# Kernel tuning notes

Measured on AMD Instinct MI355X. Metric: run time of the kernel, lower is better.

Reference implementation:

```python
import jax, jax.numpy as jnp
import numpy as np

VOCAB, D_MODEL, NHEAD, NLAYER, DIM_FF, MAX_LEN = 32000, 1024, 16, 6, 4096, 1024
B, L = 8, 1024
PAD_ID = 0
EPS = 1e-5


def _ln(x, g, b):
    m = x.mean(-1, keepdims=True)
    v = x.var(-1, keepdims=True)
    return (x - m) / jnp.sqrt(v + EPS) * g + b


def _mha(x, Wqkv, bqkv, Wo, bo, kpm):
    # x: [B,L,D]; Wqkv: [3D,D]; kpm: [B,L] bool (True = padded key)
    Bx, Lx, D = x.shape
    dh = D // NHEAD
    qkv = x @ Wqkv.T + bqkv                       # [B,L,3D]
    q, k, v = jnp.split(qkv, 3, axis=-1)
    sp = lambda t: t.reshape(Bx, Lx, NHEAD, dh).transpose(0, 2, 1, 3)  # [B,H,L,dh]
    q, k, v = sp(q), sp(k), sp(v)
    scores = jnp.einsum('bhqd,bhkd->bhqk', q, k) * (dh ** -0.5)
    scores = jnp.where(kpm[:, None, None, :], jnp.asarray(-1e9, scores.dtype), scores)
    attn = jax.nn.softmax(scores, axis=-1)        # explicit weights, as ForceWeightsMHA demands
    o = jnp.einsum('bhqk,bhkd->bhqd', attn, v)
    o = o.transpose(0, 2, 1, 3).reshape(Bx, Lx, D)
    return o @ Wo.T + bo


def setup_inputs() -> dict:
    key = jax.random.key(0)
    ks = jax.random.split(key, 20)
    s = 0.02
    n = lambda k, shp: (jax.random.normal(k, shp, dtype=jnp.float32) * s)
    inp = {
        'input_ids': jax.random.randint(ks[0], (B, L), 0, VOCAB, dtype=jnp.int64) if jax.config.jax_enable_x64 else jax.random.randint(ks[0], (B, L), 0, VOCAB).astype(jnp.int32),
        'tok_emb': n(ks[1], (VOCAB, D_MODEL)),
        'pos_emb': n(ks[2], (MAX_LEN, D_MODEL)),
        'Wqkv': n(ks[3], (NLAYER, 3 * D_MODEL, D_MODEL)),
        'bqkv': jnp.zeros((NLAYER, 3 * D_MODEL), jnp.float32),
        'Wo': n(ks[4], (NLAYER, D_MODEL, D_MODEL)),
        'bo': jnp.zeros((NLAYER, D_MODEL), jnp.float32),
        'ln1_g': jnp.ones((NLAYER, D_MODEL), jnp.float32),
        'ln1_b': jnp.zeros((NLAYER, D_MODEL), jnp.float32),
        'W1': n(ks[5], (NLAYER, DIM_FF, D_MODEL)),
        'b1': jnp.zeros((NLAYER, DIM_FF), jnp.float32),
        'W2': n(ks[6], (NLAYER, D_MODEL, DIM_FF)),
        'b2': jnp.zeros((NLAYER, D_MODEL), jnp.float32),
        'ln2_g': jnp.ones((NLAYER, D_MODEL), jnp.float32),
        'ln2_b': jnp.zeros((NLAYER, D_MODEL), jnp.float32),
        'head_ln_g': jnp.ones((D_MODEL,), jnp.float32),
        'head_ln_b': jnp.zeros((D_MODEL,), jnp.float32),
        'head_W': n(ks[7], (MAX_LEN, D_MODEL)),
        'head_b': jnp.zeros((MAX_LEN,), jnp.float32),
    }
    return inp


def reference(input_ids, tok_emb, pos_emb, Wqkv, bqkv, Wo, bo, ln1_g, ln1_b,
              W1, b1, W2, b2, ln2_g, ln2_b, head_ln_g, head_ln_b, head_W, head_b):
    Bx, Lx = input_ids.shape
    x = tok_emb[input_ids] + pos_emb[None, :Lx]           # [B,L,D]
    kpm = (input_ids == PAD_ID).at[:, 0].set(False)        # key padding mask, col 0 forced valid
    for i in range(NLAYER):                                # post-norm encoder layer (PyTorch default)
        x = _ln(x + _mha(x, Wqkv[i], bqkv[i], Wo[i], bo[i], kpm), ln1_g[i], ln1_b[i])
        ff = jax.nn.gelu(x @ W1[i].T + b1[i], approximate=False) @ W2[i].T + b2[i]
        x = _ln(x + ff, ln2_g[i], ln2_b[i])
    cls = x[:, 0, :]                                       # [B,D]
    return _ln(cls, head_ln_g, head_ln_b) @ head_W.T + head_b  # [B,MAX_LEN]
```

## Files before the change

### kernel.cpp

```cpp
#include <hip/hip_runtime.h>
#include <cstdint>

#define D_MODEL 1024
#define NHEAD   16
#define NLAYER  6
#define DIM_FF  4096
#define SEQ_B   8
#define SEQ_L   1024
#define TOKENS  (SEQ_B*SEQ_L)

typedef __bf16 v8bf  __attribute__((ext_vector_type(8)));
typedef __bf16 v4bf  __attribute__((ext_vector_type(4)));
typedef float  v4f   __attribute__((ext_vector_type(4)));

__device__ __forceinline__ void gl_lds16(const void* g, void* l) {
  __builtin_amdgcn_global_load_lds(
      (const __attribute__((address_space(1))) void*)g,
      (__attribute__((address_space(3))) void*)l, 16, 0, 0);
}

__global__ __launch_bounds__(256) void f2b_kernel(const float4* __restrict__ in,
                                                  ushort4* __restrict__ out, long n4) {
  long i = (long)blockIdx.x * 256 + threadIdx.x;
  long stride = (long)gridDim.x * 256;
  for (; i < n4; i += stride) {
    float4 v = in[i];
    v4bf r = { (__bf16)v.x, (__bf16)v.y, (__bf16)v.z, (__bf16)v.w };
    out[i] = *(ushort4*)&r;
  }
}

__global__ __launch_bounds__(256) void embed_kernel(const int* __restrict__ ids,
    const float4* __restrict__ tok, const float4* __restrict__ pos,
    float4* __restrict__ X, ushort4* __restrict__ Xb) {
  long i = (long)blockIdx.x * 256 + threadIdx.x;
  int d4 = (int)(i & 255);
  long bl = i >> 8;
  int l = (int)(bl & (SEQ_L - 1));
  int id = ids[bl];
  float4 t = tok[(long)id * 256 + d4];
  float4 p = pos[(long)l * 256 + d4];
  float4 v = {t.x + p.x, t.y + p.y, t.z + p.z, t.w + p.w};
  X[i] = v;
  v4bf r = { (__bf16)v.x, (__bf16)v.y, (__bf16)v.z, (__bf16)v.w };
  Xb[i] = *(ushort4*)&r;
}

__global__ __launch_bounds__(256) void maskb_kernel(const int* __restrict__ ids,
                                                    float* __restrict__ mb) {
  int i = blockIdx.x * 256 + threadIdx.x;
  mb[i] = (ids[i] == 0 && (i & 1023) != 0) ? -1e9f : 0.f;
}

template<int EPI>
__global__ __launch_bounds__(256) void gemm128(
    const unsigned short* __restrict__ A,
    const unsigned short* __restrict__ W,
    const float* __restrict__ bias,
    const float* __restrict__ Res,
    float* __restrict__ Cf, unsigned short* __restrict__ Cb,
    unsigned short* __restrict__ Vt,
    int M, int N, int K) {
  __shared__ unsigned short As[2 * 128 * 32];
  __shared__ unsigned short Bs[2 * 128 * 32];
  int tid = threadIdx.x;
  int wave = tid >> 6, lane = tid & 63;
  int l15 = lane & 15, quad = lane >> 4;

  int id = blockIdx.y * gridDim.x + blockIdx.x;
  int xcd = id & 7, sidx = id >> 3;
  int mt = xcd * 8 + (sidx & 7);
  int nt = sidx >> 3;
  int m0 = mt * 128, n0 = nt * 128;
  int wm = (wave >> 1) * 64, wn = (wave & 1) * 64;

  int srow = tid >> 2;
  int ssl  = (tid & 3) ^ ((srow >> 1) & 3);
  int sc8  = ssl << 3;
  const unsigned short* Ag0 = A + (long)(m0 + srow) * K + sc8;
  const unsigned short* Ag1 = A + (long)(m0 + srow + 64) * K + sc8;
  const unsigned short* Wg0 = W + (long)(n0 + srow) * K + sc8;
  const unsigned short* Wg1 = W + (long)(n0 + srow + 64) * K + sc8;
  unsigned short* As0 = As + tid * 8;
  unsigned short* Bs0 = Bs + tid * 8;

  const unsigned short* afp[4];
  const unsigned short* bfp[4];
  #pragma unroll
  for (int i = 0; i < 4; ++i) {
    int r = wm + i * 16 + l15;
    afp[i] = &As[r * 32 + ((quad ^ ((r >> 1) & 3)) << 3)];
    int rb = wn + i * 16 + l15;
    bfp[i] = &Bs[rb * 32 + ((quad ^ ((rb >> 1) & 3)) << 3)];
  }

  v4f acc[4][4];
  #pragma unroll
  for (int i = 0; i < 4; ++i)
    #pragma unroll
    for (int j = 0; j < 4; ++j) acc[i][j] = (v4f){0.f, 0.f, 0.f, 0.f};

  auto compute = [&](int bo) {
    v8bf af[4], bb[4];
    #pragma unroll
    for (int i = 0; i < 4; ++i) af[i] = *(const v8bf*)(afp[i] + bo);
    #pragma unroll
    for (int j = 0; j < 4; ++j) bb[j] = *(const v8bf*)(bfp[j] + bo);
    #pragma unroll
    for (int i = 0; i < 4; ++i)
      #pragma unroll
      for (int j = 0; j < 4; ++j)
        acc[i][j] = __builtin_amdgcn_mfma_f32_16x16x32_bf16(af[i], bb[j], acc[i][j], 0, 0, 0);
  };

  gl_lds16(Ag0, As0);
  gl_lds16(Ag1, As0 + 2048);
  gl_lds16(Wg0, Bs0);
  gl_lds16(Wg1, Bs0 + 2048);

  int ksteps = K >> 5;
  for (int ks = 0; ks < ksteps; ks += 2) {
    __syncthreads();
    {
      int k1 = (ks + 1) << 5;
      gl_lds16(Ag0 + k1, As0 + 4096);
      gl_lds16(Ag1 + k1, As0 + 6144);
      gl_lds16(Wg0 + k1, Bs0 + 4096);
      gl_lds16(Wg1 + k1, Bs0 + 6144);
    }
    compute(0);
    __syncthreads();
    if (ks + 2 < ksteps) {
      int k2 = (ks + 2) << 5;
      gl_lds16(Ag0 + k2, As0);
      gl_lds16(Ag1 + k2, As0 + 2048);
      gl_lds16(Wg0 + k2, Bs0);
      gl_lds16(Wg1 + k2, Bs0 + 2048);
    }
    compute(4096);
  }

  #pragma unroll
  for (int i = 0; i < 4; ++i) {
    int crow0 = m0 + wm + i * 16 + quad * 4;
    #pragma unroll
    for (int j = 0; j < 4; ++j) {
      int col = n0 + wn + j * 16 + l15;
      float bv = bias[col];
      if (EPI == 3 && col >= 2048) {
        int hc = (col - 2048) >> 6, d = (col - 2048) & 63;
        int bb2 = crow0 >> 10, l = crow0 & 1023;
        v4bf pk = { (__bf16)(acc[i][j][0] + bv), (__bf16)(acc[i][j][1] + bv),
                    (__bf16)(acc[i][j][2] + bv), (__bf16)(acc[i][j][3] + bv) };
        *(ushort4*)&Vt[((long)((bb2 * 16 + hc) * 64 + d)) * 1024 + l] = *(ushort4*)&pk;
      } else {
        #pragma unroll
        for (int r = 0; r < 4; ++r) {
          float v = acc[i][j][r] + bv;
          long idx = (long)(crow0 + r) * N + col;
          if (EPI == 1) {
            float u = v * (0.7978845608028654f + 0.03567740814f * v * v);
            float e = __builtin_amdgcn_exp2f(u * 2.885390081777927f);
            float th = 1.f - 2.f / (e + 1.f);
            v = 0.5f * v * (1.f + th);
          }
          if (EPI == 0) Cf[idx] = v + Res[idx];
          else          ((__bf16*)Cb)[idx] = (__bf16)v;
        }
      }
    }
  }
}

#define PSP 72
__global__ __launch_bounds__(256) void attn2(
    const unsigned short* __restrict__ QKVb,
    const unsigned short* __restrict__ Vtg,
    const float* __restrict__ mb,
    unsigned short* __restrict__ Ob) {
  __shared__ unsigned short Ks[2 * 64 * 64];
  __shared__ unsigned short Vs[2 * 64 * 64];
  __shared__ unsigned short Ps[4][16 * PSP];
  int tid = threadIdx.x, wave = tid >> 6, lane = tid & 63;
  int l15 = lane & 15, quad = lane >> 4;
  int b = blockIdx.z, h = blockIdx.y, q0 = blockIdx.x * 128;

  v8bf gq[2][2];
  #pragma unroll
  for (int t = 0; t < 2; ++t) {
    int qrow = q0 + t * 64 + wave * 16 + l15;
    const unsigned short* qb = QKVb + (long)(b * 1024 + qrow) * 3072 + h * 64;
    gq[t][0] = *(const v8bf*)(qb + quad * 8);
    gq[t][1] = *(const v8bf*)(qb + 32 + quad * 8);
  }

  v8bf bones;
  #pragma unroll
  for (int j = 0; j < 8; ++j) bones[j] = (l15 == 0) ? (__bf16)1.0f : (__bf16)0.0f;

  float m_run[2][4], l_run[2][4];
  v4f O[2][4];
  #pragma unroll
  for (int t = 0; t < 2; ++t)
    #pragma unroll
    for (int r = 0; r < 4; ++r) {
      m_run[t][r] = -1e30f; l_run[t][r] = 0.f;
      O[t][r] = (v4f){0.f, 0.f, 0.f, 0.f};
    }

  const unsigned short* kgb = QKVb + (long)b * 1024 * 3072 + 1024 + h * 64;
  const unsigned short* vgb = Vtg + (long)((b * 16 + h) * 64) * 1024;
  const float* mrow = mb + b * 1024;

  int srow = tid >> 3;
  int ssl  = (tid & 7) ^ (srow & 7);
  int ph0 = (quad ^ (l15 & 7)) << 3;
  int ph1 = ((quad + 4) ^ (l15 & 7)) << 3;
  const float SC = 0.18033688011112042f;

  gl_lds16(kgb + (long)srow * 3072 + ssl * 8, &Ks[tid * 8]);
  gl_lds16(kgb + (long)(srow + 32) * 3072 + ssl * 8, &Ks[tid * 8 + 2048]);
  gl_lds16(vgb + (long)srow * 1024 + ssl * 8, &Vs[tid * 8]);
  gl_lds16(vgb + (long)(srow + 32) * 1024 + ssl * 8, &Vs[tid * 8 + 2048]);

  for (int c = 0; c < 16; ++c) {
    int cbo = (c & 1) * 4096;
    __syncthreads();
    if (c + 1 < 16) {
      int nbo = 4096 - cbo;
      int k0n = (c + 1) * 64;
      gl_lds16(kgb + (long)(k0n + srow) * 3072 + ssl * 8, &Ks[nbo + tid * 8]);
      gl_lds16(kgb + (long)(k0n + srow + 32) * 3072 + ssl * 8, &Ks[nbo + tid * 8 + 2048]);
      gl_lds16(vgb + (long)srow * 1024 + k0n + ssl * 8, &Vs[nbo + tid * 8]);
      gl_lds16(vgb + (long)(srow + 32) * 1024 + k0n + ssl * 8, &Vs[nbo + tid * 8 + 2048]);
    }
    int k0 = c * 64;

    v8bf kf0[4], kf1[4];
    #pragma unroll
    for (int t = 0; t < 4; ++t) {
      kf0[t] = *(const v8bf*)&Ks[cbo + (t * 16 + l15) * 64 + ph0];
      kf1[t] = *(const v8bf*)&Ks[cbo + (t * 16 + l15) * 64 + ph1];
    }
    float mbv[4];
    #pragma unroll
    for (int t = 0; t < 4; ++t) mbv[t] = mrow[k0 + t * 16 + l15];

    #pragma unroll
    for (int tt = 0; tt < 2; ++tt) {
      float p[4][4], mr[4];
      #pragma unroll
      for (int r = 0; r < 4; ++r) mr[r] = -1e30f;
      #pragma unroll
      for (int t = 0; t < 4; ++t) {
        v4f s = (v4f){0.f, 0.f, 0.f, 0.f};
        s = __builtin_amdgcn_mfma_f32_16x16x32_bf16(gq[tt][0], kf0[t], s, 0, 0, 0);
        s = __builtin_amdgcn_mfma_f32_16x16x32_bf16(gq[tt][1], kf1[t], s, 0, 0, 0);
        #pragma unroll
        for (int r = 0; r < 4; ++r) {
          float sv = fmaf(s[r], SC, mbv[t]);
          p[t][r] = sv;
          mr[r] = fmaxf(mr[r], sv);
        }
      }
      #pragma unroll
      for (int r = 0; r < 4; ++r) {
        mr[r] = fmaxf(mr[r], __shfl_xor(mr[r], 1, 64));
        mr[r] = fmaxf(mr[r], __shfl_xor(mr[r], 2, 64));
        mr[r] = fmaxf(mr[r], __shfl_xor(mr[r], 4, 64));
        mr[r] = fmaxf(mr[r], __shfl_xor(mr[r], 8, 64));
      }
      float alpha[4];
      #pragma unroll
      for (int r = 0; r < 4; ++r) {
        float mn = fmaxf(m_run[tt][r], mr[r]);
        alpha[r] = __builtin_amdgcn_exp2f(m_run[tt][r] - mn);
        m_run[tt][r] = mn;
      }
      #pragma unroll
      for (int t = 0; t < 4; ++t)
        #pragma unroll
        for (int r = 0; r < 4; ++r)
          p[t][r] = __builtin_amdgcn_exp2f(p[t][r] - m_run[tt][r]);

      #pragma unroll
      for (int t = 0; t < 4; ++t)
        #pragma unroll
        for (int r = 0; r < 4; ++r)
          ((__bf16*)Ps[wave])[(quad * 4 + r) * PSP + t * 16 + l15] = (__bf16)p[t][r];
      v8bf pa0 = *(const v8bf*)&Ps[wave][l15 * PSP + quad * 8];
      v8bf pa1 = *(const v8bf*)&Ps[wave][l15 * PSP + 32 + quad * 8];

      v4f ss = (v4f){0.f, 0.f, 0.f, 0.f};
      ss = __builtin_amdgcn_mfma_f32_16x16x32_bf16(pa0, bones, ss, 0, 0, 0);
      ss = __builtin_amdgcn_mfma_f32_16x16x32_bf16(pa1, bones, ss, 0, 0, 0);

      #pragma unroll
      for (int j = 0; j < 4; ++j)
        #pragma unroll
        for (int r = 0; r < 4; ++r) O[tt][j >= 0 ? j : j][r] *= (j == 0 ? alpha[r] : 1.f);
      #pragma unroll
      for (int j = 1; j < 4; ++j)
        #pragma unroll
        for (int r = 0; r < 4; ++r) O[tt][j][r] *= alpha[r];

      #pragma unroll
      for (int j = 0; j < 4; ++j) {
        v8bf vf0 = *(const v8bf*)&Vs[cbo + (j * 16 + l15) * 64 + ph0];
        v8bf vf1 = *(const v8bf*)&Vs[cbo + (j * 16 + l15) * 64 + ph1];
        O[tt][j] = __builtin_amdgcn_mfma_f32_16x16x32_bf16(pa0, vf0, O[tt][j], 0, 0, 0);
        O[tt][j] = __builtin_amdgcn_mfma_f32_16x16x32_bf16(pa1, vf1, O[tt][j], 0, 0, 0);
      }
      #pragma unroll
      for (int r = 0; r < 4; ++r)
        l_run[tt][r] = l_run[tt][r] * alpha[r] + __shfl(ss[r], quad << 4, 64);
    }
  }

  #pragma unroll
  for (int tt = 0; tt < 2; ++tt) {
    int qd = q0 + tt * 64 + wave * 16 + quad * 4;
    #pragma unroll
    for (int r = 0; r < 4; ++r) {
      float inv = 1.f / l_run[tt][r];
      #pragma unroll
      for (int j = 0; j < 4; ++j)
        ((__bf16*)Ob)[(long)(b * 1024 + qd + r) * 1024 + h * 64 + j * 16 + l15] =
            (__bf16)(O[tt][j][r] * inv);
    }
  }
}

__global__ __launch_bounds__(256) void add_ln(
    const float* __restrict__ Xin, const float* __restrict__ Yin,
    const float* __restrict__ g, const float* __restrict__ bta,
    float* __restrict__ outF, unsigned short* __restrict__ outB,
    long in_stride, long out_stride) {
  int row = blockIdx.x;
  const float* x = Xin + (long)row * in_stride;
  const float* y = Yin ? Yin + (long)row * 1024 : nullptr;
  int tid = threadIdx.x;
  float v[4];
  float s = 0.f, s2 = 0.f;
  #pragma unroll
  for (int j = 0; j < 4; ++j) {
    int d = j * 256 + tid;
    float t = x[d] + (y ? y[d] : 0.f);
    v[j] = t; s += t; s2 += t * t;
  }
  __shared__ float red[8];
  int lane = tid & 63, wave = tid >> 6;
  #pragma unroll
  for (int o = 32; o > 0; o >>= 1) { s += __shfl_down(s, o, 64); s2 += __shfl_down(s2, o, 64); }
  if (lane == 0) { red[wave] = s; red[4 + wave] = s2; }
  __syncthreads();
  s  = red[0] + red[1] + red[2] + red[3];
  s2 = red[4] + red[5] + red[6] + red[7];
  float mean = s * (1.f / 1024.f);
  float var  = s2 * (1.f / 1024.f) - mean * mean;
  float rstd = rsqrtf(var + 1e-5f);
  float* of = outF + (long)row * out_stride;
  unsigned short* ob = outB ? outB + (long)row * out_stride : nullptr;
  #pragma unroll
  for (int j = 0; j < 4; ++j) {
    int d = j * 256 + tid;
    float o = (v[j] - mean) * rstd * g[d] + bta[d];
    of[d] = o;
    if (ob) ((__bf16*)ob)[d] = (__bf16)o;
  }
}

__global__ __launch_bounds__(256) void head_kernel(
    const float* __restrict__ cls, const float* __restrict__ hW,
    const float* __restrict__ hb, float* __restrict__ out) {
  int n = blockIdx.x * 256 + threadIdx.x;
  int b = blockIdx.y;
  const float4* c4 = (const float4*)(cls + b * 1024);
  const float4* w4 = (const float4*)(hW + (long)n * 1024);
  float s = 0.f;
  #pragma unroll 8
  for (int d = 0; d < 256; ++d) {
    float4 a = c4[d], w = w4[d];
    s += a.x * w.x + a.y * w.y + a.z * w.z + a.w * w.w;
  }
  out[b * 1024 + n] = s + hb[n];
}

extern "C" void kernel_launch(void* const* d_in, const int* in_sizes, int n_in,
                              void* d_out, int out_size, void* d_ws, size_t ws_size,
                              hipStream_t stream) {
  const int*   ids  = (const int*)d_in[0];
  const float* tok  = (const float*)d_in[1];
  const float* pos  = (const float*)d_in[2];
  const float* Wqkv = (const float*)d_in[3];
  const float* bqkv = (const float*)d_in[4];
  const float* Wo   = (const float*)d_in[5];
  const float* bo   = (const float*)d_in[6];
  const float* ln1g = (const float*)d_in[7];
  const float* ln1b = (const float*)d_in[8];
  const float* W1   = (const float*)d_in[9];
  const float* b1   = (const float*)d_in[10];
  const float* W2   = (const float*)d_in[11];
  const float* b2   = (const float*)d_in[12];
  const float* ln2g = (const float*)d_in[13];
  const float* ln2b = (const float*)d_in[14];
  const float* hlng = (const float*)d_in[15];
  const float* hlnb = (const float*)d_in[16];
  const float* hW   = (const float*)d_in[17];
  const float* hb   = (const float*)d_in[18];
  float* out = (float*)d_out;

  char* ws = (char*)d_ws;
  size_t off = 0;
  auto alloc = [&](size_t bytes) {
    char* p = ws + off;
    off = (off + bytes + 255) & ~(size_t)255;
    return p;
  };
  unsigned short* Wqkv_b = (unsigned short*)alloc((size_t)NLAYER*3072*1024*2);
  unsigned short* Wo_b   = (unsigned short*)alloc((size_t)NLAYER*1024*1024*2);
  unsigned short* W1_b   = (unsigned short*)alloc((size_t)NLAYER*4096*1024*2);
  unsigned short* W2_b   = (unsigned short*)alloc((size_t)NLAYER*1024*4096*2);
  float*          X      = (float*)alloc((size_t)TOKENS*1024*4);
  unsigned short* Xb     = (unsigned short*)alloc((size_t)TOKENS*1024*2);
  unsigned short* Qb     = (unsigned short*)alloc((size_t)TOKENS*3072*2);
  unsigned short* Vtg    = (unsigned short*)alloc((size_t)TOKENS*1024*2);
  float*          Y      = (float*)alloc((size_t)TOKENS*1024*4);
  unsigned short* Ab     = (unsigned short*)alloc((size_t)TOKENS*1024*2);
  unsigned short* Gb     = Qb;
  float*          cls    = (float*)alloc(8*1024*4);
  float*          mb     = (float*)alloc(TOKENS*4);

  f2b_kernel<<<2048, 256, 0, stream>>>((const float4*)Wqkv, (ushort4*)Wqkv_b, (long)NLAYER*3072*1024/4);
  f2b_kernel<<<2048, 256, 0, stream>>>((const float4*)Wo,   (ushort4*)Wo_b,   (long)NLAYER*1024*1024/4);
  f2b_kernel<<<2048, 256, 0, stream>>>((const float4*)W1,   (ushort4*)W1_b,   (long)NLAYER*4096*1024/4);
  f2b_kernel<<<2048, 256, 0, stream>>>((const float4*)W2,   (ushort4*)W2_b,   (long)NLAYER*1024*4096/4);
  embed_kernel<<<(TOKENS*256)/256, 256, 0, stream>>>(ids, (const float4*)tok, (const float4*)pos,
                                                     (float4*)X, (ushort4*)Xb);
  maskb_kernel<<<TOKENS/256, 256, 0, stream>>>(ids, mb);

  for (int i = 0; i < NLAYER; ++i) {
    gemm128<3><<<dim3(3072/128, TOKENS/128), 256, 0, stream>>>(
        Xb, Wqkv_b + (size_t)i*3072*1024, bqkv + i*3072, nullptr, nullptr, Qb, Vtg, TOKENS, 3072, 1024);
    attn2<<<dim3(SEQ_L/128, NHEAD, SEQ_B), 256, 0, stream>>>(Qb, Vtg, mb, Ab);
    gemm128<0><<<dim3(1024/128, TOKENS/128), 256, 0, stream>>>(
        Ab, Wo_b + (size_t)i*1024*1024, bo + i*1024, X, Y, nullptr, nullptr, TOKENS, 1024, 1024);
    add_ln<<<TOKENS, 256, 0, stream>>>(Y, nullptr, ln1g + i*1024, ln1b + i*1024, X, Xb, 1024L, 1024L);
    gemm128<1><<<dim3(4096/128, TOKENS/128), 256, 0, stream>>>(
        Xb, W1_b + (size_t)i*4096*1024, b1 + i*4096, nullptr, nullptr, Gb, nullptr, TOKENS, 4096, 1024);
    gemm128<0><<<dim3(1024/128, TOKENS/128), 256, 0, stream>>>(
        Gb, W2_b + (size_t)i*1024*4096, b2 + i*1024, X, Y, nullptr, nullptr, TOKENS, 1024, 4096);
    add_ln<<<TOKENS, 256, 0, stream>>>(Y, nullptr, ln2g + i*1024, ln2b + i*1024, X, Xb, 1024L, 1024L);
  }
  add_ln<<<8, 256, 0, stream>>>(X, nullptr, hlng, hlnb, cls, nullptr, (long)SEQ_L*1024, 1024L);
  head_kernel<<<dim3(4, 8), 256, 0, stream>>>(cls, hW, hb, out);
}
```

Baseline: 3.402 ms.

## Drop LDS staging in GEMM and attention, load MFMA operands directly from global

Both the GEMM and the attention kernel stop staging tiles through double-buffered shared memory via global_load_lds, and each wave now reads its MFMA fragments straight from global memory (relying on L1/L2 for reuse). This removes the block-wide barriers and LDS traffic. In exchange, data shared between waves of a block is fetched redundantly from cache, the row-strided 16-byte loads are poorly coalesced, and there is no explicit prefetch to hide global latency. That is likely to make the GEMMs memory-latency bound.

```diff
diff --git a/kernel.cpp b/kernel.cpp
--- a/kernel.cpp
+++ b/kernel.cpp
@@ -12,12 +12,6 @@
 typedef __bf16 v8bf  __attribute__((ext_vector_type(8)));
 typedef __bf16 v4bf  __attribute__((ext_vector_type(4)));
 typedef float  v4f   __attribute__((ext_vector_type(4)));
-
-__device__ __forceinline__ void gl_lds16(const void* g, void* l) {
-  __builtin_amdgcn_global_load_lds(
-      (const __attribute__((address_space(1))) void*)g,
-      (__attribute__((address_space(3))) void*)l, 16, 0, 0);
-}
 
 __global__ __launch_bounds__(256) void f2b_kernel(const float4* __restrict__ in,
                                                   ushort4* __restrict__ out, long n4) {
@@ -53,7 +47,7 @@
 }
 
 template<int EPI>
-__global__ __launch_bounds__(256) void gemm128(
+__global__ __launch_bounds__(256) void gemmd(
     const unsigned short* __restrict__ A,
     const unsigned short* __restrict__ W,
     const float* __restrict__ bias,
@@ -61,8 +55,6 @@
     float* __restrict__ Cf, unsigned short* __restrict__ Cb,
     unsigned short* __restrict__ Vt,
     int M, int N, int K) {
-  __shared__ unsigned short As[2 * 128 * 32];
-  __shared__ unsigned short Bs[2 * 128 * 32];
   int tid = threadIdx.x;
   int wave = tid >> 6, lane = tid & 63;
   int l15 = lane & 15, quad = lane >> 4;
@@ -74,24 +66,12 @@
   int m0 = mt * 128, n0 = nt * 128;
   int wm = (wave >> 1) * 64, wn = (wave & 1) * 64;
 
-  int srow = tid >> 2;
-  int ssl  = (tid & 3) ^ ((srow >> 1) & 3);
-  int sc8  = ssl << 3;
-  const unsigned short* Ag0 = A + (long)(m0 + srow) * K + sc8;
-  const unsigned short* Ag1 = A + (long)(m0 + srow + 64) * K + sc8;
-  const unsigned short* Wg0 = W + (long)(n0 + srow) * K + sc8;
-  const unsigned short* Wg1 = W + (long)(n0 + srow + 64) * K + sc8;
-  unsigned short* As0 = As + tid * 8;
-  unsigned short* Bs0 = Bs + tid * 8;
-
-  const unsigned short* afp[4];
-  const unsigned short* bfp[4];
+  const unsigned short* Ap[4];
+  const unsigned short* Bp[4];
   #pragma unroll
   for (int i = 0; i < 4; ++i) {
-    int r = wm + i * 16 + l15;
-    afp[i] = &As[r * 32 + ((quad ^ ((r >> 1) & 3)) << 3)];
-    int rb = wn + i * 16 + l15;
-    bfp[i] = &Bs[rb * 32 + ((quad ^ ((rb >> 1) & 3)) << 3)];
+    Ap[i] = A + (long)(m0 + wm + i * 16 + l15) * K + quad * 8;
+    Bp[i] = W + (long)(n0 + wn + i * 16 + l15) * K + quad * 8;
   }
 
   v4f acc[4][4];
@@ -100,44 +80,18 @@
     #pragma unroll
     for (int j = 0; j < 4; ++j) acc[i][j] = (v4f){0.f, 0.f, 0.f, 0.f};
 
-  auto compute = [&](int bo) {
-    v8bf af[4], bb[4];
-    #pragma unroll
-    for (int i = 0; i < 4; ++i) af[i] = *(const v8bf*)(afp[i] + bo);
-    #pragma unroll
-    for (int j = 0; j < 4; ++j) bb[j] = *(const v8bf*)(bfp[j] + bo);
+  #pragma unroll 4
+  for (int k = 0; k < K; k += 32) {
+    v8bf af[4], bf[4];
+    #pragma unroll
+    for (int i = 0; i < 4; ++i) af[i] = *(const v8bf*)(Ap[i] + k);
+    #pragma unroll
+    for (int j = 0; j < 4; ++j) bf[j] = *(const v8bf*)(Bp[j] + k);
     #pragma unroll
     for (int i = 0; i < 4; ++i)
       #pragma unroll
       for (int j = 0; j < 4; ++j)
-        acc[i][j] = __builtin_amdgcn_mfma_f32_16x16x32_bf16(af[i], bb[j], acc[i][j], 0, 0, 0);
-  };
-
-  gl_lds16(Ag0, As0);
-  gl_lds16(Ag1, As0 + 2048);
-  gl_lds16(Wg0, Bs0);
-  gl_lds16(Wg1, Bs0 + 2048);
-
-  int ksteps = K >> 5;
-  for (int ks = 0; ks < ksteps; ks += 2) {
-    __syncthreads();
-    {
-      int k1 = (ks + 1) << 5;
-      gl_lds16(Ag0 + k1, As0 + 4096);
-      gl_lds16(Ag1 + k1, As0 + 6144);
-      gl_lds16(Wg0 + k1, Bs0 + 4096);
-      gl_lds16(Wg1 + k1, Bs0 + 6144);
-    }
-    compute(0);
-    __syncthreads();
-    if (ks + 2 < ksteps) {
-      int k2 = (ks + 2) << 5;
-      gl_lds16(Ag0 + k2, As0);
-      gl_lds16(Ag1 + k2, As0 + 2048);
-      gl_lds16(Wg0 + k2, Bs0);
-      gl_lds16(Wg1 + k2, Bs0 + 2048);
-    }
-    compute(4096);
+        acc[i][j] = __builtin_amdgcn_mfma_f32_16x16x32_bf16(af[i], bf[j], acc[i][j], 0, 0, 0);
   }
 
   #pragma unroll
@@ -178,8 +132,6 @@
     const unsigned short* __restrict__ Vtg,
     const float* __restrict__ mb,
     unsigned short* __restrict__ Ob) {
-  __shared__ unsigned short Ks[2 * 64 * 64];
-  __shared__ unsigned short Vs[2 * 64 * 64];
   __shared__ unsigned short Ps[4][16 * PSP];
   int tid = threadIdx.x, wave = tid >> 6, lane = tid & 63;
   int l15 = lane & 15, quad = lane >> 4;
@@ -210,41 +162,35 @@
 
   const unsigned short* kgb = QKVb + (long)b * 1024 * 3072 + 1024 + h * 64;
   const unsigned short* vgb = Vtg + (long)((b * 16 + h) * 64) * 1024;
+  const unsigned short* Kp[4];
+  const unsigned short* Vp[4];
+  #pragma unroll
+  for (int t = 0; t < 4; ++t) {
+    Kp[t] = kgb + (long)(t * 16 + l15) * 3072 + quad * 8;
+    Vp[t] = vgb + (long)(t * 16 + l15) * 1024 + quad * 8;
+  }
   const float* mrow = mb + b * 1024;
-
-  int srow = tid >> 3;
-  int ssl  = (tid & 7) ^ (srow & 7);
-  int ph0 = (quad ^ (l15 & 7)) << 3;
-  int ph1 = ((quad + 4) ^ (l15 & 7)) << 3;
   const float SC = 0.18033688011112042f;
 
-  gl_lds16(kgb + (long)srow * 3072 + ssl * 8, &Ks[tid * 8]);
-  gl_lds16(kgb + (long)(srow + 32) * 3072 + ssl * 8, &Ks[tid * 8 + 2048]);
-  gl_lds16(vgb + (long)srow * 1024 + ssl * 8, &Vs[tid * 8]);
-  gl_lds16(vgb + (long)(srow + 32) * 1024 + ssl * 8, &Vs[tid * 8 + 2048]);
-
   for (int c = 0; c < 16; ++c) {
-    int cbo = (c & 1) * 4096;
-    __syncthreads();
-    if (c + 1 < 16) {
-      int nbo = 4096 - cbo;
-      int k0n = (c + 1) * 64;
-      gl_lds16(kgb + (long)(k0n + srow) * 3072 + ssl * 8, &Ks[nbo + tid * 8]);
-      gl_lds16(kgb + (long)(k0n + srow + 32) * 3072 + ssl * 8, &Ks[nbo + tid * 8 + 2048]);
-      gl_lds16(vgb + (long)srow * 1024 + k0n + ssl * 8, &Vs[nbo + tid * 8]);
-      gl_lds16(vgb + (long)(srow + 32) * 1024 + k0n + ssl * 8, &Vs[nbo + tid * 8 + 2048]);
-    }
     int k0 = c * 64;
-
     v8bf kf0[4], kf1[4];
     #pragma unroll
     for (int t = 0; t < 4; ++t) {
-      kf0[t] = *(const v8bf*)&Ks[cbo + (t * 16 + l15) * 64 + ph0];
-      kf1[t] = *(const v8bf*)&Ks[cbo + (t * 16 + l15) * 64 + ph1];
+      const unsigned short* kp = Kp[t] + (long)k0 * 3072;
+      kf0[t] = *(const v8bf*)kp;
+      kf1[t] = *(const v8bf*)(kp + 32);
     }
     float mbv[4];
     #pragma unroll
     for (int t = 0; t < 4; ++t) mbv[t] = mrow[k0 + t * 16 + l15];
+
+    v8bf vf0[4], vf1[4];
+    #pragma unroll
+    for (int j = 0; j < 4; ++j) {
+      vf0[j] = *(const v8bf*)(Vp[j] + k0);
+      vf1[j] = *(const v8bf*)(Vp[j] + k0 + 32);
+    }
 
     #pragma unroll
     for (int tt = 0; tt < 2; ++tt) {
@@ -298,18 +244,12 @@
       #pragma unroll
       for (int j = 0; j < 4; ++j)
         #pragma unroll
-        for (int r = 0; r < 4; ++r) O[tt][j >= 0 ? j : j][r] *= (j == 0 ? alpha[r] : 1.f);
-      #pragma unroll
-      for (int j = 1; j < 4; ++j)
-        #pragma unroll
         for (int r = 0; r < 4; ++r) O[tt][j][r] *= alpha[r];
 
       #pragma unroll
       for (int j = 0; j < 4; ++j) {
-        v8bf vf0 = *(const v8bf*)&Vs[cbo + (j * 16 + l15) * 64 + ph0];
-        v8bf vf1 = *(const v8bf*)&Vs[cbo + (j * 16 + l15) * 64 + ph1];
-        O[tt][j] = __builtin_amdgcn_mfma_f32_16x16x32_bf16(pa0, vf0, O[tt][j], 0, 0, 0);
-        O[tt][j] = __builtin_amdgcn_mfma_f32_16x16x32_bf16(pa1, vf1, O[tt][j], 0, 0, 0);
+        O[tt][j] = __builtin_amdgcn_mfma_f32_16x16x32_bf16(pa0, vf0[j], O[tt][j], 0, 0, 0);
+        O[tt][j] = __builtin_amdgcn_mfma_f32_16x16x32_bf16(pa1, vf1[j], O[tt][j], 0, 0, 0);
       }
       #pragma unroll
       for (int r = 0; r < 4; ++r)
@@ -440,15 +380,15 @@
   maskb_kernel<<<TOKENS/256, 256, 0, stream>>>(ids, mb);
 
   for (int i = 0; i < NLAYER; ++i) {
-    gemm128<3><<<dim3(3072/128, TOKENS/128), 256, 0, stream>>>(
+    gemmd<3><<<dim3(3072/128, TOKENS/128), 256, 0, stream>>>(
         Xb, Wqkv_b + (size_t)i*3072*1024, bqkv + i*3072, nullptr, nullptr, Qb, Vtg, TOKENS, 3072, 1024);
     attn2<<<dim3(SEQ_L/128, NHEAD, SEQ_B), 256, 0, stream>>>(Qb, Vtg, mb, Ab);
-    gemm128<0><<<dim3(1024/128, TOKENS/128), 256, 0, stream>>>(
+    gemmd<0><<<dim3(1024/128, TOKENS/128), 256, 0, stream>>>(
         Ab, Wo_b + (size_t)i*1024*1024, bo + i*1024, X, Y, nullptr, nullptr, TOKENS, 1024, 1024);
     add_ln<<<TOKENS, 256, 0, stream>>>(Y, nullptr, ln1g + i*1024, ln1b + i*1024, X, Xb, 1024L, 1024L);
-    gemm128<1><<<dim3(4096/128, TOKENS/128), 256, 0, stream>>>(
+    gemmd<1><<<dim3(4096/128, TOKENS/128), 256, 0, stream>>>(
         Xb, W1_b + (size_t)i*4096*1024, b1 + i*4096, nullptr, nullptr, Gb, nullptr, TOKENS, 4096, 1024);
-    gemm128<0><<<dim3(1024/128, TOKENS/128), 256, 0, stream>>>(
+    gemmd<0><<<dim3(1024/128, TOKENS/128), 256, 0, stream>>>(
         Gb, W2_b + (size_t)i*1024*4096, b2 + i*1024, X, Y, nullptr, nullptr, TOKENS, 1024, 4096);
     add_ln<<<TOKENS, 256, 0, stream>>>(Y, nullptr, ln2g + i*1024, ln2b + i*1024, X, Xb, 1024L, 1024L);
   }
```

After: 5.664 ms. 66.5% more time.
